# Performance work log

Measured on AMD Instinct MI355X. Metric: run time of the kernel, lower is better.

The kernel has to match this reference:

```python
import jax, jax.numpy as jnp
import numpy as np

EPS = 1e-6      # torch F.pairwise_distance default eps (added to the difference)
MARGIN = 1.0

def _cdist_eps(a, b):
    # Exact ||a_i - b_j + eps||_2 via expansion:
    # ||a-b+eps||^2 = ||a||^2 + ||b||^2 - 2 a.b + 2*eps*(sum(a)-sum(b)) + D*eps^2
    D = a.shape[-1]
    sq = (jnp.sum(a * a, axis=1)[:, None]
          + jnp.sum(b * b, axis=1)[None, :]
          - 2.0 * (a @ b.T)
          + 2.0 * EPS * (jnp.sum(a, axis=1)[:, None] - jnp.sum(b, axis=1)[None, :])
          + D * EPS * EPS)
    return jnp.sqrt(jnp.maximum(sq, 0.0))

def setup_inputs() -> dict:
    key = jax.random.key(0)
    k1, k2, k3 = jax.random.split(key, 3)
    B, D = 4096, 1024
    return {
        'anchor_embeddings': jax.random.normal(k1, (B, D), dtype=jnp.float32),
        'positive_embeddings': jax.random.normal(k2, (B, D), dtype=jnp.float32),
        'negative_embeddings': jax.random.normal(k3, (B, D), dtype=jnp.float32),
    }

def reference(anchor_embeddings, positive_embeddings, negative_embeddings):
    a, p, n = anchor_embeddings, positive_embeddings, negative_embeddings
    # per-row anchor-positive and anchor-negative distances
    d_ap = jnp.linalg.norm(a - p + EPS, axis=-1)          # [B]
    d_an_row = jnp.linalg.norm(a - n + EPS, axis=-1)      # [B]

    # hardest negative: for each anchor, max over negatives with dist < d_ap[i], else 0
    dan_mat = _cdist_eps(a, n)                            # [B, B]
    mask_n = dan_mat < d_ap[:, None]
    hard_n = jnp.where(mask_n.any(axis=1),
                       jnp.max(jnp.where(mask_n, dan_mat, -jnp.inf), axis=1),
                       0.0)
    d_an = jnp.mean(hard_n)                               # scalar

    # hardest positive: for each anchor, min over positives with dist > d(a_i, n_i), else 0
    dpp_mat = _cdist_eps(a, p)                            # [B, B]
    mask_p = dpp_mat > d_an_row[:, None]
    hard_p = jnp.where(mask_p.any(axis=1),
                       jnp.min(jnp.where(mask_p, dpp_mat, jnp.inf), axis=1),
                       0.0)
    d_pp = jnp.mean(hard_p)                               # scalar

    loss = jnp.mean(jnp.clip(d_ap - 0.5 * d_pp - 0.5 * d_an + MARGIN, 0.0, None))
    return loss
```

## Files before the change

### kernel.cpp

```cpp
#include <hip/hip_runtime.h>


#define NB 4096
#define DIM 1024
#define EPSF 1e-6f
#define D_EPS2 (1024.0f * 1e-6f * 1e-6f)

#define BM 128
#define BK 64

typedef __bf16  bf16x8 __attribute__((ext_vector_type(8)));
typedef float   f32x4  __attribute__((ext_vector_type(4)));

__device__ __forceinline__ unsigned short f2bf(float x) {
    unsigned u = __float_as_uint(x);
    u += 0x7FFFu + ((u >> 16) & 1u);
    return (unsigned short)(u >> 16);
}

__device__ __forceinline__ void g2l16(const unsigned short* g, unsigned short* l) {
    __builtin_amdgcn_global_load_lds(
        (const __attribute__((address_space(1))) unsigned int*)g,
        (__attribute__((address_space(3))) unsigned int*)l, 16, 0, 0);
}

#define FENCE    asm volatile("" ::: "memory")
#define VM4      asm volatile("s_waitcnt vmcnt(4)" ::: "memory")
#define VM12     asm volatile("s_waitcnt vmcnt(12)" ::: "memory")
#define VM0      asm volatile("s_waitcnt vmcnt(0)" ::: "memory")
#define BARRIER  asm volatile("s_barrier" ::: "memory")


__global__ __launch_bounds__(256) void row_stats_kernel(
    const float* __restrict__ a, const float* __restrict__ p,
    const float* __restrict__ n,
    unsigned short* __restrict__ abf, unsigned short* __restrict__ pbf,
    unsigned short* __restrict__ nbf, float* __restrict__ stats)
{
    const int t    = threadIdx.x;
    const int wave = t >> 6, lane = t & 63;
    const int row  = blockIdx.x * 4 + wave;
    const size_t base = (size_t)row * DIM;

    const float4* a4 = (const float4*)(a + base);
    const float4* p4 = (const float4*)(p + base);
    const float4* n4 = (const float4*)(n + base);

    float v[8] = {0,0,0,0,0,0,0,0};
#pragma unroll
    for (int c = 0; c < 4; c++) {
        const int idx = c * 64 + lane;
        const float4 va = a4[idx];
        const float4 vp = p4[idx];
        const float4 vn = n4[idx];
        const float fa[4] = {va.x, va.y, va.z, va.w};
        const float fp[4] = {vp.x, vp.y, vp.z, vp.w};
        const float fn[4] = {vn.x, vn.y, vn.z, vn.w};
#pragma unroll
        for (int e = 0; e < 4; e++) {
            v[0] += fa[e];           v[1] += fa[e] * fa[e];
            v[2] += fp[e];           v[3] += fp[e] * fp[e];
            v[4] += fn[e];           v[5] += fn[e] * fn[e];
            float dp = fa[e] - fp[e] + EPSF;  v[6] += dp * dp;
            float dn = fa[e] - fn[e] + EPSF;  v[7] += dn * dn;
        }
        ushort4 ba, bp, bn;
        ba.x = f2bf(fa[0]); ba.y = f2bf(fa[1]); ba.z = f2bf(fa[2]); ba.w = f2bf(fa[3]);
        bp.x = f2bf(fp[0]); bp.y = f2bf(fp[1]); bp.z = f2bf(fp[2]); bp.w = f2bf(fp[3]);
        bn.x = f2bf(fn[0]); bn.y = f2bf(fn[1]); bn.z = f2bf(fn[2]); bn.w = f2bf(fn[3]);
        ((ushort4*)(abf + base))[idx] = ba;
        ((ushort4*)(pbf + base))[idx] = bp;
        ((ushort4*)(nbf + base))[idx] = bn;
    }

#pragma unroll
    for (int m = 32; m >= 1; m >>= 1)
#pragma unroll
        for (int q = 0; q < 8; q++) v[q] += __shfl_xor(v[q], m);

    if (lane == 0) {
        stats[0 * NB + row] = v[1] + 2.0f * EPSF * v[0] + D_EPS2;
        stats[1 * NB + row] = v[5] - 2.0f * EPSF * v[4];
        stats[2 * NB + row] = v[3] - 2.0f * EPSF * v[2];
        stats[3 * NB + row] = sqrtf(v[6]);
        stats[4 * NB + row] = sqrtf(v[7]);
        ((unsigned*)stats)[5 * NB + row] = 0u;
        ((unsigned*)stats)[6 * NB + row] = 0x7f800000u;
    }
}

__global__ __launch_bounds__(256, 2) void gemm_mask_kernel(
    const unsigned short* __restrict__ Abf,
    const unsigned short* __restrict__ Nbf,
    const unsigned short* __restrict__ Pbf,
    float* __restrict__ stats)
{
    const int id = blockIdx.y * 32 + blockIdx.x;
    const int xc = id & 7, rr = id >> 3;
    const int j0 = (xc * 4 + (rr & 3)) * BM;
    const int i0 = (rr >> 2) * BM;

    __shared__ unsigned short sN[2][BM * BK];
    __shared__ unsigned short sP[2][BM * BK];

    const int t    = threadIdx.x;
    const int wave = t >> 6, lane = t & 63;
    const int wm   = wave >> 1, wn = wave & 1;
    const int quad = lane >> 4, lrow = lane & 15;

    const int srow = lane >> 3;
    const int kch  = ((lane & 7) ^ srow) * 8;
    const unsigned short* gN = Nbf + (size_t)(j0 + wave * 32 + srow) * DIM + kch;
    const unsigned short* gP = Pbf + (size_t)(j0 + wave * 32 + srow) * DIM + kch;
    const int lb = (wave * 32) * BK;

    const unsigned short* gA = Abf + (size_t)(i0 + wm * 64 + lrow) * DIM + (quad << 3);

    const int rsw0 = ((0 + quad) ^ (lrow & 7)) * 8;
    const int rsw1 = ((4 + quad) ^ (lrow & 7)) * 8;
    const int pboff = (wn * 64 + lrow) * BK;

    bf16x8 afr0[4], afr1[4];
    f32x4 accN[4][4], accP[4][4];
#pragma unroll
    for (int im = 0; im < 4; im++)
#pragma unroll
        for (int jn = 0; jn < 4; jn++) {
            accN[im][jn] = (f32x4)(0.0f);
            accP[im][jn] = (f32x4)(0.0f);
        }

#define ISSUE_B(kw_, b_) do {                                                 \
    const unsigned short* _gn = gN + (size_t)(kw_) * BK;                      \
    const unsigned short* _gp = gP + (size_t)(kw_) * BK;                      \
    unsigned short* _ln = &sN[(b_)][lb];                                      \
    unsigned short* _lp = &sP[(b_)][lb];                                      \
    _Pragma("unroll")                                                         \
    for (int g = 0; g < 4; g++) {                                             \
        g2l16(_gn + (size_t)g * 8 * DIM, _ln + g * 8 * BK);                   \
        g2l16(_gp + (size_t)g * 8 * DIM, _lp + g * 8 * BK);                   \
    }                                                                         \
} while (0)

#define ISSUE_A(kw_, h_, arr_) do {                                           \
    const unsigned short* _ga = gA + (size_t)(kw_) * BK + (h_) * 32;          \
    _Pragma("unroll")                                                         \
    for (int im = 0; im < 4; im++)                                            \
        arr_[im] = *(const bf16x8*)(_ga + im * 16 * DIM);                     \
} while (0)

#define COMPUTE_HALF(b_, rsw_, arr_) do {                                     \
    bf16x8 bnfr[4], bpfr[4];                                                  \
    _Pragma("unroll")                                                         \
    for (int jn = 0; jn < 4; jn++) {                                          \
        bnfr[jn] = *(const bf16x8*)(&sN[(b_)][pboff + jn * 16 * BK + (rsw_)]);\
        bpfr[jn] = *(const bf16x8*)(&sP[(b_)][pboff + jn * 16 * BK + (rsw_)]);\
    }                                                                         \
    _Pragma("unroll")                                                         \
    for (int im = 0; im < 4; im++)                                            \
        _Pragma("unroll")                                                     \
        for (int jn = 0; jn < 4; jn++) {                                      \
            accN[im][jn] = __builtin_amdgcn_mfma_f32_16x16x32_bf16(           \
                arr_[im], bnfr[jn], accN[im][jn], 0, 0, 0);                   \
            accP[im][jn] = __builtin_amdgcn_mfma_f32_16x16x32_bf16(           \
                arr_[im], bpfr[jn], accP[im][jn], 0, 0, 0);                   \
        }                                                                     \
} while (0)

    ISSUE_B(0, 0);      FENCE;
    ISSUE_A(0, 0, afr0); FENCE;
    ISSUE_A(0, 1, afr1); FENCE;

    for (int k = 0; k < 15; k++) {
        const int b = k & 1;
        VM4;
        BARRIER;
        ISSUE_B(k + 1, b ^ 1); FENCE;
        COMPUTE_HALF(b, rsw0, afr0);
        ISSUE_A(k + 1, 0, afr0); FENCE;
        VM12;
        COMPUTE_HALF(b, rsw1, afr1);
        ISSUE_A(k + 1, 1, afr1); FENCE;
    }
    VM4;
    BARRIER;
    COMPUTE_HALF(1, rsw0, afr0);
    VM0;
    COMPUTE_HALF(1, rsw1, afr1);

#undef COMPUTE_HALF
#undef ISSUE_A
#undef ISSUE_B

    const float* __restrict__ base_a = stats + 0 * NB;
    const float* __restrict__ cn_v   = stats + 1 * NB;
    const float* __restrict__ cp_v   = stats + 2 * NB;
    const float* __restrict__ d_ap   = stats + 3 * NB;
    const float* __restrict__ d_an   = stats + 4 * NB;
    unsigned* __restrict__ hard_n = ((unsigned*)stats) + 5 * NB;
    unsigned* __restrict__ hard_p = ((unsigned*)stats) + 6 * NB;

#pragma unroll
    for (int im = 0; im < 4; im++) {
#pragma unroll
        for (int r = 0; r < 4; r++) {
            const int gi = i0 + wm * 64 + im * 16 + quad * 4 + r;
            const float cutN = d_ap[gi];
            const float cutP = d_an[gi];
            const float cutN2 = cutN * cutN;
            const float cutP2 = cutP * cutP;
            const float bi    = base_a[gi];
            float bestN = 0.0f;
            float bestP = __uint_as_float(0x7f800000u);
#pragma unroll
            for (int jn = 0; jn < 4; jn++) {
                const int gj = j0 + wn * 64 + jn * 16 + lrow;
                const float sqN = fmaxf(bi + cn_v[gj] - 2.0f * accN[im][jn][r], 0.0f);
                const float sqP = fmaxf(bi + cp_v[gj] - 2.0f * accP[im][jn][r], 0.0f);
                if (sqN < cutN2 && sqN > bestN) bestN = sqN;
                if (sqP > cutP2 && sqP < bestP) bestP = sqP;
            }
#pragma unroll
            for (int m = 1; m < 16; m <<= 1) {
                bestN = fmaxf(bestN, __shfl_xor(bestN, m));
                bestP = fminf(bestP, __shfl_xor(bestP, m));
            }
            if (lrow == 0) {
                const unsigned bn_ = __float_as_uint(bestN);
                const unsigned bp_ = __float_as_uint(bestP);
                if (bn_ != 0u)          atomicMax(hard_n + gi, bn_);
                if (bp_ != 0x7f800000u) atomicMin(hard_p + gi, bp_);
            }
        }
    }
}

__global__ __launch_bounds__(1024) void finalize_kernel(
    const float* __restrict__ stats, float* __restrict__ out)
{
    const unsigned* hard_n = ((const unsigned*)stats) + 5 * NB;
    const unsigned* hard_p = ((const unsigned*)stats) + 6 * NB;
    const float*    d_ap   = stats + 3 * NB;
    const int t = threadIdx.x;
    const int wave = t >> 6, lane = t & 63;
    __shared__ float pn[16], pp[16];
    __shared__ float s_dan, s_dpp;

    float sn = 0.0f, sp = 0.0f;
    for (int i = t; i < NB; i += 1024) {
        sn += sqrtf(__uint_as_float(hard_n[i]));
        const unsigned hp = hard_p[i];
        if (hp != 0x7f800000u) sp += sqrtf(__uint_as_float(hp));
    }
#pragma unroll
    for (int m = 32; m >= 1; m >>= 1) {
        sn += __shfl_xor(sn, m);
        sp += __shfl_xor(sp, m);
    }
    if (lane == 0) { pn[wave] = sn; pp[wave] = sp; }
    __syncthreads();
    if (t == 0) {
        float an = 0.0f, ap = 0.0f;
#pragma unroll
        for (int w = 0; w < 16; w++) { an += pn[w]; ap += pp[w]; }
        s_dan = an / (float)NB;
        s_dpp = ap / (float)NB;
    }
    __syncthreads();
    const float dan = s_dan, dpp = s_dpp;

    float accv = 0.0f;
    for (int i = t; i < NB; i += 1024)
        accv += fmaxf(d_ap[i] - 0.5f * dpp - 0.5f * dan + 1.0f, 0.0f);
#pragma unroll
    for (int m = 32; m >= 1; m >>= 1) accv += __shfl_xor(accv, m);
    if (lane == 0) pn[wave] = accv;
    __syncthreads();
    if (t == 0) {
        float s = 0.0f;
#pragma unroll
        for (int w = 0; w < 16; w++) s += pn[w];
        out[0] = s / (float)NB;
    }
}

extern "C" void kernel_launch(void* const* d_in, const int* in_sizes, int n_in,
                              void* d_out, int out_size, void* d_ws, size_t ws_size,
                              hipStream_t stream) {
    const float* a = (const float*)d_in[0];
    const float* p = (const float*)d_in[1];
    const float* n = (const float*)d_in[2];
    float* out = (float*)d_out;

    unsigned short* abf = (unsigned short*)d_ws;
    unsigned short* pbf = abf + (size_t)NB * DIM;
    unsigned short* nbf = pbf + (size_t)NB * DIM;
    float* stats = (float*)(nbf + (size_t)NB * DIM);

    row_stats_kernel<<<NB / 4, 256, 0, stream>>>(a, p, n, abf, pbf, nbf, stats);

    dim3 grid(NB / BM, NB / BM);
    gemm_mask_kernel<<<grid, 256, 0, stream>>>(abf, nbf, pbf, stats);

    finalize_kernel<<<1, 1024, 0, stream>>>(stats, out);
}
```

Before: 196.2 us.

## Give each wave a private 128x32 B slice to drop the block barrier

Changes the wave tiling from a 2x2 grid of 64x64 tiles to four 128x32 column strips. Each wave now consumes only the B rows it staged into LDS itself, so the per-iteration s_barrier is removed and the vmcnt thresholds are retuned for the new load counts. In exchange, every wave loads all 128 A rows from global memory, doubling per-wave A fragment loads and A register use, which raises global traffic and register pressure.

```diff
diff --git a/kernel.cpp b/kernel.cpp
--- a/kernel.cpp
+++ b/kernel.cpp
@@ -25,10 +25,9 @@
 }
 
 #define FENCE    asm volatile("" ::: "memory")
-#define VM4      asm volatile("s_waitcnt vmcnt(4)" ::: "memory")
-#define VM12     asm volatile("s_waitcnt vmcnt(12)" ::: "memory")
+#define VM8      asm volatile("s_waitcnt vmcnt(8)" ::: "memory")
+#define VM16     asm volatile("s_waitcnt vmcnt(16)" ::: "memory")
 #define VM0      asm volatile("s_waitcnt vmcnt(0)" ::: "memory")
-#define BARRIER  asm volatile("s_barrier" ::: "memory")
 
 
 __global__ __launch_bounds__(256) void row_stats_kernel(
@@ -105,7 +104,6 @@
 
     const int t    = threadIdx.x;
     const int wave = t >> 6, lane = t & 63;
-    const int wm   = wave >> 1, wn = wave & 1;
     const int quad = lane >> 4, lrow = lane & 15;
 
     const int srow = lane >> 3;
@@ -114,18 +112,18 @@
     const unsigned short* gP = Pbf + (size_t)(j0 + wave * 32 + srow) * DIM + kch;
     const int lb = (wave * 32) * BK;
 
-    const unsigned short* gA = Abf + (size_t)(i0 + wm * 64 + lrow) * DIM + (quad << 3);
+    const unsigned short* gA = Abf + (size_t)(i0 + lrow) * DIM + (quad << 3);
 
     const int rsw0 = ((0 + quad) ^ (lrow & 7)) * 8;
     const int rsw1 = ((4 + quad) ^ (lrow & 7)) * 8;
-    const int pboff = (wn * 64 + lrow) * BK;
-
-    bf16x8 afr0[4], afr1[4];
-    f32x4 accN[4][4], accP[4][4];
-#pragma unroll
-    for (int im = 0; im < 4; im++)
-#pragma unroll
-        for (int jn = 0; jn < 4; jn++) {
+    const int pboff = (wave * 32 + lrow) * BK;
+
+    bf16x8 afr0[8], afr1[8];
+    f32x4 accN[8][2], accP[8][2];
+#pragma unroll
+    for (int im = 0; im < 8; im++)
+#pragma unroll
+        for (int jn = 0; jn < 2; jn++) {
             accN[im][jn] = (f32x4)(0.0f);
             accP[im][jn] = (f32x4)(0.0f);
         }
@@ -145,21 +143,21 @@
 #define ISSUE_A(kw_, h_, arr_) do {                                           \
     const unsigned short* _ga = gA + (size_t)(kw_) * BK + (h_) * 32;          \
     _Pragma("unroll")                                                         \
-    for (int im = 0; im < 4; im++)                                            \
+    for (int im = 0; im < 8; im++)                                            \
         arr_[im] = *(const bf16x8*)(_ga + im * 16 * DIM);                     \
 } while (0)
 
-#define COMPUTE_HALF(b_, rsw_, arr_) do {                                     \
-    bf16x8 bnfr[4], bpfr[4];                                                  \
+#define HALF(b_, rsw_, arr_) do {                                             \
+    bf16x8 bnfr[2], bpfr[2];                                                  \
     _Pragma("unroll")                                                         \
-    for (int jn = 0; jn < 4; jn++) {                                          \
+    for (int jn = 0; jn < 2; jn++) {                                          \
         bnfr[jn] = *(const bf16x8*)(&sN[(b_)][pboff + jn * 16 * BK + (rsw_)]);\
         bpfr[jn] = *(const bf16x8*)(&sP[(b_)][pboff + jn * 16 * BK + (rsw_)]);\
     }                                                                         \
     _Pragma("unroll")                                                         \
-    for (int im = 0; im < 4; im++)                                            \
+    for (int im = 0; im < 8; im++)                                            \
         _Pragma("unroll")                                                     \
-        for (int jn = 0; jn < 4; jn++) {                                      \
+        for (int jn = 0; jn < 2; jn++) {                                      \
             accN[im][jn] = __builtin_amdgcn_mfma_f32_16x16x32_bf16(           \
                 arr_[im], bnfr[jn], accN[im][jn], 0, 0, 0);                   \
             accP[im][jn] = __builtin_amdgcn_mfma_f32_16x16x32_bf16(           \
@@ -167,28 +165,32 @@
         }                                                                     \
 } while (0)
 
-    ISSUE_B(0, 0);      FENCE;
+#define WINDOW(k_, b_) do {                                                   \
+    VM8;                                          \
+    ISSUE_B((k_) + 1, (b_) ^ 1); FENCE;                                       \
+    HALF((b_), rsw0, afr0);                                                   \
+    ISSUE_A((k_) + 1, 0, afr0); FENCE;                                        \
+    VM16;                                                \
+    HALF((b_), rsw1, afr1);                                                   \
+    ISSUE_A((k_) + 1, 1, afr1); FENCE;                                        \
+} while (0)
+
+    ISSUE_B(0, 0); FENCE;
     ISSUE_A(0, 0, afr0); FENCE;
     ISSUE_A(0, 1, afr1); FENCE;
 
-    for (int k = 0; k < 15; k++) {
-        const int b = k & 1;
-        VM4;
-        BARRIER;
-        ISSUE_B(k + 1, b ^ 1); FENCE;
-        COMPUTE_HALF(b, rsw0, afr0);
-        ISSUE_A(k + 1, 0, afr0); FENCE;
-        VM12;
-        COMPUTE_HALF(b, rsw1, afr1);
-        ISSUE_A(k + 1, 1, afr1); FENCE;
-    }
-    VM4;
-    BARRIER;
-    COMPUTE_HALF(1, rsw0, afr0);
+    for (int kp = 0; kp < 7; kp++) {
+        WINDOW(2 * kp,     0);
+        WINDOW(2 * kp + 1, 1);
+    }
+    WINDOW(14, 0);
+    VM8;
+    HALF(1, rsw0, afr0);
     VM0;
-    COMPUTE_HALF(1, rsw1, afr1);
-
-#undef COMPUTE_HALF
+    HALF(1, rsw1, afr1);
+
+#undef WINDOW
+#undef HALF
 #undef ISSUE_A
 #undef ISSUE_B
 
@@ -201,10 +203,10 @@
     unsigned* __restrict__ hard_p = ((unsigned*)stats) + 6 * NB;
 
 #pragma unroll
-    for (int im = 0; im < 4; im++) {
+    for (int im = 0; im < 8; im++) {
 #pragma unroll
         for (int r = 0; r < 4; r++) {
-            const int gi = i0 + wm * 64 + im * 16 + quad * 4 + r;
+            const int gi = i0 + im * 16 + quad * 4 + r;
             const float cutN = d_ap[gi];
             const float cutP = d_an[gi];
             const float cutN2 = cutN * cutN;
@@ -213,8 +215,8 @@
             float bestN = 0.0f;
             float bestP = __uint_as_float(0x7f800000u);
 #pragma unroll
-            for (int jn = 0; jn < 4; jn++) {
-                const int gj = j0 + wn * 64 + jn * 16 + lrow;
+            for (int jn = 0; jn < 2; jn++) {
+                const int gj = j0 + wave * 32 + jn * 16 + lrow;
                 const float sqN = fmaxf(bi + cn_v[gj] - 2.0f * accN[im][jn][r], 0.0f);
                 const float sqP = fmaxf(bi + cp_v[gj] - 2.0f * accP[im][jn][r], 0.0f);
                 if (sqN < cutN2 && sqN > bestN) bestN = sqN;
```

Result: slower. 296.3 us (+51.0%).
